# Kernel optimization log

Hardware: AMD Instinct MI355X
Metric: run time of the kernel (lower is better)

## Reference

```python
import jax, jax.numpy as jnp
import numpy as np

RES = 32  # voxel grid resolution per axis (cfg.MODEL.NEURAL_POINTS.VOXEL_RES)


def upsample_ac(x, s):
    """Bilinear upsample with align_corners=True. x: [B,C,h,w] -> [B,C,h*s,w*s]."""
    if s == 1:
        return x
    B, C, h, w = x.shape
    H, W = h * s, w * s
    ys = jnp.arange(H, dtype=x.dtype) * ((h - 1) / (H - 1))
    xs = jnp.arange(W, dtype=x.dtype) * ((w - 1) / (W - 1))
    y0 = jnp.floor(ys).astype(jnp.int32)
    x0 = jnp.floor(xs).astype(jnp.int32)
    y1 = jnp.minimum(y0 + 1, h - 1)
    x1 = jnp.minimum(x0 + 1, w - 1)
    wy = (ys - y0.astype(x.dtype))[:, None]  # [H,1]
    wx = (xs - x0.astype(x.dtype))[None, :]  # [1,W]
    top = x[:, :, y0, :]
    bot = x[:, :, y1, :]
    a = top[..., x0]; b = top[..., x1]; c = bot[..., x0]; d = bot[..., x1]
    return (a * (1 - wx) + b * wx) * (1 - wy) + (c * (1 - wx) + d * wx) * wy


def vox_closest(pos):
    """construct_vox_points_closest: per occupied voxel, index of point closest to
    the voxel's point centroid. pos: [N,3] -> [RES^3] int32 indices."""
    N = pos.shape[0]
    Vn = RES ** 3
    mn = pos.min(0)
    mx = pos.max(0)
    vsz = (mx - mn) / RES  # obtain_voxel_size_based_grid_res
    coord = jnp.clip(jnp.floor((pos - mn) / vsz).astype(jnp.int32), 0, RES - 1)
    vid = (coord[:, 0] * RES + coord[:, 1]) * RES + coord[:, 2]  # [N]
    cnt = jax.ops.segment_sum(jnp.ones((N,), pos.dtype), vid, Vn)
    cen = jax.ops.segment_sum(pos, vid, Vn) / jnp.maximum(cnt, 1.0)[:, None]
    d = jnp.sum((pos - cen[vid]) ** 2, axis=-1)  # [N] dist^2 to own-voxel centroid
    dmin = jax.ops.segment_min(d, vid, Vn)
    cand = jnp.where(d <= dmin[vid], jnp.arange(N, dtype=jnp.int32), N)
    midx = jax.ops.segment_min(cand, vid, Vn)
    return jnp.where(midx >= N, 0, midx)  # guard (rare) empty voxels


def reference(rgb, f1, f2, f3, points_pos, points_dir, W1, b1, W2, b2, points_mask):
    V, _, H, W = rgb.shape
    N = V * H * W
    C = 59
    # valid_index = where(points_mask == 1) (mask is all ones -> identity gather)
    valid = jnp.nonzero(points_mask[0] == 1, size=N, fill_value=0)[0]
    pos = points_pos[0, valid]          # [N,3]
    pdir = points_dir[0, valid]         # [N,3]
    # project_point_feats: upsample each pyramid level to full res, concat channels
    ups = [upsample_ac(rgb, 1), upsample_ac(f1, 2), upsample_ac(f2, 4), upsample_ac(f3, 8)]
    pif = jnp.concatenate(ups, axis=1)                       # [V,59,H,W]
    pif = jnp.transpose(pif, (0, 2, 3, 1)).reshape(N, C)     # [N,59]
    color = jax.lax.stop_gradient(jnp.transpose(rgb, (0, 2, 3, 1)).reshape(N, 3))
    pif = pif[valid]
    color = color[valid]
    emb = jnp.concatenate([pif, pdir], axis=-1)              # [N,62]
    midx = vox_closest(pos)                                  # [32768]
    sel_emb = emb[midx]
    sel_pos = pos[midx]
    sel_color = color[midx]
    sel_dir = pdir[midx]
    # point_mlp (premlp_init): 62 -> 256 -> 256
    h = jax.nn.relu(sel_emb @ W1 + b1)
    points_embedding = h @ W2 + b2
    return points_embedding, sel_pos, sel_color, sel_dir


def setup_inputs() -> dict:
    key = jax.random.key(0)
    ks = jax.random.split(key, 10)
    V, H, W = 8, 240, 320
    N = V * H * W
    return {
        "rgb": jax.random.uniform(ks[0], (V, 3, H, W), jnp.float32),
        "f1": jax.random.normal(ks[1], (V, 8, H // 2, W // 2), jnp.float32),
        "f2": jax.random.normal(ks[2], (V, 16, H // 4, W // 4), jnp.float32),
        "f3": jax.random.normal(ks[3], (V, 32, H // 8, W // 8), jnp.float32),
        "points_pos": jax.random.uniform(ks[4], (1, N, 3), jnp.float32),
        "points_dir": jax.random.normal(ks[5], (1, N, 3), jnp.float32),
        "W1": jax.random.normal(ks[6], (62, 256), jnp.float32) * 0.05,
        "b1": jnp.zeros((256,), jnp.float32),
        "W2": jax.random.normal(ks[7], (256, 256), jnp.float32) * 0.05,
        "b2": jnp.zeros((256,), jnp.float32),
        "points_mask": jnp.ones((1, N), jnp.int32),
    }
```

## Files before the change

kernel.cpp:

```cpp
#include <hip/hip_runtime.h>
#include <hip/hip_bf16.h>
#include <limits.h>
#include <stddef.h>

#define NPTS   614400
#define RESV   32
#define NVOX   (RESV*RESV*RESV)
#define IMG_H  240
#define IMG_W  320
#define IMG_HW (IMG_H*IMG_W)
#define INF    __builtin_inff()
#define CAP    64
#define CAPP   32
#define SPILLCAP 4096
#define NBKT   128
#define BCAP   6144
#define BOVFCAP 4096

typedef __attribute__((ext_vector_type(8))) short short8;
typedef __attribute__((ext_vector_type(4))) short s16x4;
typedef __attribute__((ext_vector_type(4))) float f32x4;
typedef float f32x4u __attribute__((ext_vector_type(4), aligned(4)));

__device__ __forceinline__ float fadd_(float a, float b){
#pragma clang fp contract(off)
  return a + b;
}
__device__ __forceinline__ float fsub_(float a, float b){
#pragma clang fp contract(off)
  return a - b;
}
__device__ __forceinline__ float fmul_(float a, float b){
#pragma clang fp contract(off)
  return a * b;
}
__device__ __forceinline__ float fdiv_(float a, float b){
#pragma clang fp contract(off)
  return a / b;
}

__device__ __forceinline__ short f2bf(float x){
  __hip_bfloat16 h = __float2bfloat16(x);
  return *reinterpret_cast<short*>(&h);
}

__global__ void k_prep(int* __restrict__ spillcnt, int* __restrict__ gbase,
                       const float* __restrict__ W1, const float* __restrict__ W2,
                       short* __restrict__ W1t, short* __restrict__ W2t,
                       const float* __restrict__ pos,
                       f32x4* __restrict__ pmin, f32x4* __restrict__ pmax){
  int gid = blockIdx.x*blockDim.x + threadIdx.x;
  int stride = gridDim.x*blockDim.x;
  if (gid == 0){ spillcnt[0] = 0; spillcnt[1] = 0; }
  if (gid < NBKT) gbase[gid] = 0;
  if (gid < 256*64){
    int n = gid >> 6, k = gid & 63;
    W1t[gid] = (k < 62) ? f2bf(W1[k*256 + n]) : (short)0;
  } else if (gid < 256*64 + 256*256){
    int j = gid - 256*64;
    int n = j >> 8, k = j & 255;
    W2t[j] = f2bf(W2[k*256 + n]);
  }

  const f32x4* p4 = (const f32x4*)pos;
  float mn[3] = {  INF,  INF,  INF };
  float mx[3] = { -INF, -INF, -INF };
  for (int t = gid; t < NPTS/4; t += stride){
    f32x4 a = p4[3*t+0], b = p4[3*t+1], c = p4[3*t+2];
    mn[0] = fminf(mn[0], fminf(fminf(a.x, a.w), fminf(b.z, c.y)));
    mx[0] = fmaxf(mx[0], fmaxf(fmaxf(a.x, a.w), fmaxf(b.z, c.y)));
    mn[1] = fminf(mn[1], fminf(fminf(a.y, b.x), fminf(b.w, c.z)));
    mx[1] = fmaxf(mx[1], fmaxf(fmaxf(a.y, b.x), fmaxf(b.w, c.z)));
    mn[2] = fminf(mn[2], fminf(fminf(a.z, b.y), fminf(c.x, c.w)));
    mx[2] = fmaxf(mx[2], fmaxf(fmaxf(a.z, b.y), fmaxf(c.x, c.w)));
  }
  #pragma unroll
  for (int off = 32; off >= 1; off >>= 1){
    #pragma unroll
    for (int c = 0; c < 3; c++){
      mn[c] = fminf(mn[c], __shfl_down(mn[c], off, 64));
      mx[c] = fmaxf(mx[c], __shfl_down(mx[c], off, 64));
    }
  }
  __shared__ float smn[4][3], smx[4][3];
  int lane = threadIdx.x & 63, w = threadIdx.x >> 6;
  if (lane == 0){
    #pragma unroll
    for (int c = 0; c < 3; c++){ smn[w][c] = mn[c]; smx[w][c] = mx[c]; }
  }
  __syncthreads();
  if (threadIdx.x == 0){
    f32x4 a, b;
    a.x = fminf(fminf(smn[0][0], smn[1][0]), fminf(smn[2][0], smn[3][0]));
    a.y = fminf(fminf(smn[0][1], smn[1][1]), fminf(smn[2][1], smn[3][1]));
    a.z = fminf(fminf(smn[0][2], smn[1][2]), fminf(smn[2][2], smn[3][2]));
    a.w = 0.f;
    b.x = fmaxf(fmaxf(smx[0][0], smx[1][0]), fmaxf(smx[2][0], smx[3][0]));
    b.y = fmaxf(fmaxf(smx[0][1], smx[1][1]), fmaxf(smx[2][1], smx[3][1]));
    b.z = fmaxf(fmaxf(smx[0][2], smx[1][2]), fmaxf(smx[2][2], smx[3][2]));
    b.w = 0.f;
    pmin[blockIdx.x] = a;
    pmax[blockIdx.x] = b;
  }
}

__device__ __forceinline__ void reduce_minmax(const f32x4* __restrict__ pmin,
                                              const f32x4* __restrict__ pmax,
                                              float mn[3], float vsz[3]){
  int t = threadIdx.x;
  f32x4 a = pmin[t], b = pmin[t+256];
  f32x4 c = pmax[t], d = pmax[t+256];
  float lmn[3] = { fminf(a.x,b.x), fminf(a.y,b.y), fminf(a.z,b.z) };
  float lmx[3] = { fmaxf(c.x,d.x), fmaxf(c.y,d.y), fmaxf(c.z,d.z) };
  #pragma unroll
  for (int off = 32; off >= 1; off >>= 1){
    #pragma unroll
    for (int k = 0; k < 3; k++){
      lmn[k] = fminf(lmn[k], __shfl_xor(lmn[k], off, 64));
      lmx[k] = fmaxf(lmx[k], __shfl_xor(lmx[k], off, 64));
    }
  }
  __shared__ float smn[4][3], smx[4][3];
  int lane = t & 63, w = t >> 6;
  if (lane == 0){
    #pragma unroll
    for (int k = 0; k < 3; k++){ smn[w][k] = lmn[k]; smx[w][k] = lmx[k]; }
  }
  __syncthreads();
  #pragma unroll
  for (int k = 0; k < 3; k++){
    mn[k] = fminf(fminf(smn[0][k], smn[1][k]), fminf(smn[2][k], smn[3][k]));
    float mx = fmaxf(fmaxf(smx[0][k], smx[1][k]), fmaxf(smx[2][k], smx[3][k]));
    vsz[k] = fdiv_(fsub_(mx, mn[k]), 32.0f);
  }
}

__global__ void k_bucket(const float* __restrict__ pos,
                         const f32x4* __restrict__ pmin, const f32x4* __restrict__ pmax,
                         int* __restrict__ gbase, f32x4* __restrict__ bucketbuf,
                         int* __restrict__ bovfcnt, f32x4* __restrict__ bovf,
                         const float* __restrict__ f1, const float* __restrict__ f2,
                         const float* __restrict__ f3,
                         float* __restrict__ f1t, float* __restrict__ f2t,
                         float* __restrict__ f3t, int tposed){
  float mn[3], vsz[3];
  reduce_minmax(pmin, pmax, mn, vsz);

  __shared__ int h[NBKT], cur[NBKT];
  int t = threadIdx.x;
  if (t < NBKT) h[t] = 0;
  __syncthreads();

  int base = blockIdx.x*blockDim.x + t;
  const f32x4* p4 = (const f32x4*)pos;
  f32x4 a = p4[3*base+0], b = p4[3*base+1], c = p4[3*base+2];
  float X[4] = {a.x, a.w, b.z, c.y};
  float Y[4] = {a.y, b.x, b.w, c.z};
  float Z[4] = {a.z, b.y, c.x, c.w};
  int vox[4];
  #pragma unroll
  for (int j = 0; j < 4; j++){
    float P[3] = {X[j], Y[j], Z[j]};
    int v = 0;
    #pragma unroll
    for (int k = 0; k < 3; k++){
      float tt = fdiv_(fsub_(P[k], mn[k]), vsz[k]);
      int cc = (int)floorf(tt);
      cc = min(max(cc, 0), RESV-1);
      v = v*RESV + cc;
    }
    vox[j] = v;
    atomicAdd(&h[v >> 8], 1);
  }
  __syncthreads();
  if (t < NBKT) cur[t] = atomicAdd(&gbase[t], h[t]);
  __syncthreads();
  #pragma unroll
  for (int j = 0; j < 4; j++){
    int i = 4*base + j;
    int bk = vox[j] >> 8;
    int r = atomicAdd(&cur[bk], 1);
    f32x4 e = { X[j], Y[j], Z[j], __int_as_float(i) };
    if (r < BCAP){
      bucketbuf[(size_t)bk*BCAP + r] = e;
    } else {
      int so = atomicAdd(bovfcnt, 1);
      if (so < BOVFCAP) bovf[so] = e;
    }
  }

  if (tposed){
    int gid = blockIdx.x*blockDim.x + t;
    int stride = gridDim.x*blockDim.x;
    for (int p = gid; p < 8*19200; p += stride){
      int img = p / 19200, pix = p - img*19200;
      const float* s = f1 + (size_t)img*8*19200 + pix;
      float r[8];
      #pragma unroll
      for (int c = 0; c < 8; c++) r[c] = s[(size_t)c*19200];
      float* d = f1t + (size_t)p*8;
      *(f32x4*)&d[0] = (f32x4){r[0],r[1],r[2],r[3]};
      *(f32x4*)&d[4] = (f32x4){r[4],r[5],r[6],r[7]};
    }
    for (int p = gid; p < 8*4800; p += stride){
      int img = p / 4800, pix = p - img*4800;
      const float* s = f2 + (size_t)img*16*4800 + pix;
      float* d = f2t + (size_t)p*16;
      #pragma unroll
      for (int cq = 0; cq < 4; cq++){
        f32x4 v = { s[(size_t)(4*cq+0)*4800], s[(size_t)(4*cq+1)*4800],
                    s[(size_t)(4*cq+2)*4800], s[(size_t)(4*cq+3)*4800] };
        *(f32x4*)&d[4*cq] = v;
      }
    }
    for (int p = gid; p < 8*1200; p += stride){
      int img = p / 1200, pix = p - img*1200;
      const float* s = f3 + (size_t)img*32*1200 + pix;
      float* d = f3t + (size_t)p*32;
      #pragma unroll
      for (int cq = 0; cq < 8; cq++){
        f32x4 v = { s[(size_t)(4*cq+0)*1200], s[(size_t)(4*cq+1)*1200],
                    s[(size_t)(4*cq+2)*1200], s[(size_t)(4*cq+3)*1200] };
        *(f32x4*)&d[4*cq] = v;
      }
    }
  }
}

__launch_bounds__(512)
__global__ void k_vox2(const f32x4* __restrict__ pmin, const f32x4* __restrict__ pmax,
                       const int* __restrict__ gbase, const f32x4* __restrict__ bucketbuf,
                       const int* __restrict__ bovfcnt, const f32x4* __restrict__ bovf,
                       int* __restrict__ cnt, int* __restrict__ slots,
                       int* __restrict__ spillcnt, int2* __restrict__ spill,
                       f32x4* __restrict__ slotpos, int haspp){
  __shared__ float smn[8][3], smx[8][3];
  __shared__ int cnt_s[256];
  int t = threadIdx.x;
  if (t < 256) cnt_s[t] = 0;

  {
    int tt = t & 255;
    f32x4 a = pmin[tt], b = pmin[tt+256];
    f32x4 c = pmax[tt], d = pmax[tt+256];
    float lmn[3] = { fminf(a.x,b.x), fminf(a.y,b.y), fminf(a.z,b.z) };
    float lmx[3] = { fmaxf(c.x,d.x), fmaxf(c.y,d.y), fmaxf(c.z,d.z) };
    #pragma unroll
    for (int off = 32; off >= 1; off >>= 1){
      #pragma unroll
      for (int k = 0; k < 3; k++){
        lmn[k] = fminf(lmn[k], __shfl_xor(lmn[k], off, 64));
        lmx[k] = fmaxf(lmx[k], __shfl_xor(lmx[k], off, 64));
      }
    }
    int lane = t & 63, w = t >> 6;
    if (lane == 0){
      #pragma unroll
      for (int k = 0; k < 3; k++){ smn[w][k] = lmn[k]; smx[w][k] = lmx[k]; }
    }
  }
  __syncthreads();
  float mn[3], vsz[3];
  #pragma unroll
  for (int k = 0; k < 3; k++){
    float lo = smn[0][k], hi = smx[0][k];
    #pragma unroll
    for (int w = 1; w < 8; w++){ lo = fminf(lo, smn[w][k]); hi = fmaxf(hi, smx[w][k]); }
    mn[k] = lo;
    vsz[k] = fdiv_(fsub_(hi, lo), 32.0f);
  }

  int b = blockIdx.x;
  int nb = min(gbase[b], BCAP);
  for (int j = t; j < nb; j += 512){
    f32x4 rec = bucketbuf[(size_t)b*BCAP + j];
    float P[3] = {rec.x, rec.y, rec.z};
    int v = 0;
    #pragma unroll
    for (int k = 0; k < 3; k++){
      float tt = fdiv_(fsub_(P[k], mn[k]), vsz[k]);
      int cc = (int)floorf(tt);
      cc = min(max(cc, 0), RESV-1);
      v = v*RESV + cc;
    }
    int p = atomicAdd(&cnt_s[v & 255], 1);
    if (haspp && p < CAPP){
      slotpos[(size_t)v*CAPP + p] = rec;
    } else if (p < CAP){
      slots[v*CAP + p] = __float_as_int(rec.w);
    } else {
      int sp = atomicAdd(spillcnt, 1);
      if (sp < SPILLCAP){ int2 e; e.x = v; e.y = __float_as_int(rec.w); spill[sp] = e; }
    }
  }
  int bc = min(*bovfcnt, BOVFCAP);
  for (int j = t; j < bc; j += 512){
    f32x4 rec = bovf[j];
    float P[3] = {rec.x, rec.y, rec.z};
    int v = 0;
    #pragma unroll
    for (int k = 0; k < 3; k++){
      float tt = fdiv_(fsub_(P[k], mn[k]), vsz[k]);
      int cc = (int)floorf(tt);
      cc = min(max(cc, 0), RESV-1);
      v = v*RESV + cc;
    }
    if ((v >> 8) == b){
      int p = atomicAdd(&cnt_s[v & 255], 1);
      if (haspp && p < CAPP){
        slotpos[(size_t)v*CAPP + p] = rec;
      } else if (p < CAP){
        slots[v*CAP + p] = __float_as_int(rec.w);
      } else {
        int sp = atomicAdd(spillcnt, 1);
        if (sp < SPILLCAP){ int2 e; e.x = v; e.y = __float_as_int(rec.w); spill[sp] = e; }
      }
    }
  }
  __syncthreads();
  if (t < 256) cnt[(b << 8) + t] = cnt_s[t];
}

__launch_bounds__(256)
__global__ void k_voxfull(const int* __restrict__ cnt, const int* __restrict__ slots,
                          const int* __restrict__ spillcnt, const int2* __restrict__ spill,
                          const f32x4* __restrict__ slotpos, int haspp,
                          const float* __restrict__ pos,
                          const float* __restrict__ pdir, const float* __restrict__ rgb,
                          const float* __restrict__ f1, const float* __restrict__ f2,
                          const float* __restrict__ f3,
                          const float* __restrict__ f1t, const float* __restrict__ f2t,
                          const float* __restrict__ f3t, int tposed,
                          float* __restrict__ selpos, float* __restrict__ selcol,
                          float* __restrict__ seldir, short* __restrict__ emb){
  __shared__ __align__(16) int skey[4][64];
  __shared__ f32x4 sposl[4][64];
  int lane = threadIdx.x & 63;
  int wv   = threadIdx.x >> 6;
  int v = blockIdx.x*4 + wv;

  f32x4 q = {0.f, 0.f, 0.f, 0.f};
  if (haspp) q = slotpos[(size_t)v*CAPP + (lane & (CAPP-1))];
  int n = cnt[v];

  int m = 0;
  unsigned long long ball = 0;
  float px = 0.f, py = 0.f, pz = 0.f;

  if (n > CAP){
    if (lane == 0){
      int sc = min(*spillcnt, SPILLCAP);
      float sx = 0.f, sy = 0.f, sz = 0.f; int last = -1;
      for (int i = 0; i < n; i++){
        int best = INT_MAX;
        for (int j = 0; j < CAP; j++){
          int id = (haspp && j < CAPP) ? __float_as_int(slotpos[(size_t)v*CAPP + j].w)
                                       : slots[v*CAP + j];
          if (id > last && id < best) best = id;
        }
        for (int j = 0; j < sc; j++){
          int2 e = spill[j];
          if (e.x == v && e.y > last && e.y < best) best = e.y;
        }
        sx = fadd_(sx, pos[3*best+0]);
        sy = fadd_(sy, pos[3*best+1]);
        sz = fadd_(sz, pos[3*best+2]);
        last = best;
      }
      float cf = (float)n;
      float cx = fdiv_(sx, cf), cy = fdiv_(sy, cf), cz = fdiv_(sz, cf);
      float dmin = INF; int mm = 0;
      for (int j = 0; j < CAP + sc; j++){
        int id; int ok = 1;
        if (j < CAP){
          id = (haspp && j < CAPP) ? __float_as_int(slotpos[(size_t)v*CAPP + j].w)
                                   : slots[v*CAP + j];
        } else { int2 e = spill[j-CAP]; ok = (e.x == v); id = e.y; }
        if (!ok) continue;
        float dx = fsub_(pos[3*id+0], cx);
        float dy = fsub_(pos[3*id+1], cy);
        float dz = fsub_(pos[3*id+2], cz);
        float d  = fadd_(fadd_(fmul_(dx,dx), fmul_(dy,dy)), fmul_(dz,dz));
        if (d < dmin || (d == dmin && id < mm)){ dmin = d; mm = id; }
      }
      m = mm;
    }
    m = __shfl(m, 0, 64);
  } else {
    int key = INT_MAX;
    if (haspp && n <= CAPP){
      if (lane < n){
        px = q.x; py = q.y; pz = q.z;
        key = __float_as_int(q.w);
      }
    } else if (haspp){
      if (lane < CAPP){
        px = q.x; py = q.y; pz = q.z;
        key = __float_as_int(q.w);
      } else if (lane < n){
        key = slots[v*CAP + lane];
        if (key < NPTS-1){
          f32x4u qq = *(const f32x4u*)&pos[3*key];
          px = qq.x; py = qq.y; pz = qq.z;
        } else {
          px = pos[3*key+0]; py = pos[3*key+1]; pz = pos[3*key+2];
        }
      }
    } else {
      if (lane < n){
        key = slots[v*CAP + lane];
        if (key < NPTS-1){
          f32x4u qq = *(const f32x4u*)&pos[3*key];
          px = qq.x; py = qq.y; pz = qq.z;
        } else {
          px = pos[3*key+0]; py = pos[3*key+1]; pz = pos[3*key+2];
        }
      }
    }

    skey[wv][lane] = key;
    __builtin_amdgcn_wave_barrier();
    int r = 0;
    {
      int nq = (n + 3) >> 2;
      const int4* k4 = (const int4*)&skey[wv][0];
      for (int j = 0; j < nq; j++){
        int4 kk = k4[j];
        r += (kk.x < key) + (kk.y < key) + (kk.z < key) + (kk.w < key);
      }
    }
    if (lane < n){
      f32x4 e = { px, py, pz, 0.f };
      sposl[wv][r] = e;
    }
    __builtin_amdgcn_wave_barrier();

    float sx = 0.f, sy = 0.f, sz = 0.f;
    for (int i = 0; i < n; i++){
      f32x4 pp = sposl[wv][i];
      sx = fadd_(sx, pp.x);
      sy = fadd_(sy, pp.y);
      sz = fadd_(sz, pp.z);
    }
    float cf = fmaxf((float)n, 1.0f);
    float cx = fdiv_(sx, cf), cy = fdiv_(sy, cf), cz = fdiv_(sz, cf);

    float bd = INF; int bi = 0;
    if (lane < n){
      float dx = fsub_(px, cx), dy = fsub_(py, cy), dz = fsub_(pz, cz);
      bd = fadd_(fadd_(fmul_(dx,dx), fmul_(dy,dy)), fmul_(dz,dz));
      bi = key;
    }
    #pragma unroll
    for (int off = 32; off >= 1; off >>= 1){
      float od = __shfl_xor(bd, off, 64);
      int   oi = __shfl_xor(bi, off, 64);
      if (od < bd || (od == bd && oi < bi)){ bd = od; bi = oi; }
    }
    m = bi;
    ball = __ballot(lane < n && key == m);
  }

  float wx_ = 0.f, wy_ = 0.f, wz_ = 0.f;
  if (ball){
    int wl = (int)(__ffsll((long long)ball) - 1);
    wx_ = __shfl(px, wl, 64);
    wy_ = __shfl(py, wl, 64);
    wz_ = __shfl(pz, wl, 64);
  }

  int img = m / IMG_HW;
  int rem = m - img*IMG_HW;
  int y = rem / IMG_W;
  int x = rem - y*IMG_W;
  int ch = lane;
  float val;
  if (ch < 3){
    val = rgb[((img*3 + ch)*IMG_H + y)*IMG_W + x];
    selcol[3*v+ch] = val;
    float sp = ball ? ((ch == 0) ? wx_ : (ch == 1) ? wy_ : wz_) : pos[3*m+ch];
    selpos[3*v+ch] = sp;
  } else if (ch < 59){
    int lvl = (ch >= 27) ? 2 : ((ch >= 11) ? 1 : 0);
    int c   = ch - ((lvl == 0) ? 3 : ((lvl == 1) ? 11 : 27));
    int C   = 8 << lvl;
    int h   = 120 >> lvl, w = 160 >> lvl;
    float ry = (lvl == 0) ? (119.0f/239.0f) : ((lvl == 1) ? (59.0f/239.0f) : (29.0f/239.0f));
    float rx = (lvl == 0) ? (159.0f/319.0f) : ((lvl == 1) ? (79.0f/319.0f) : (39.0f/319.0f));
    float ys = (float)y * ry;
    float xs = (float)x * rx;
    int y0 = (int)floorf(ys);
    int x0 = (int)floorf(xs);
    int y1 = min(y0+1, h-1);
    int x1 = min(x0+1, w-1);
    float wy = ys - (float)y0;
    float wx = xs - (float)x0;
    float aa, bb, cc, dd;
    if (tposed){
      const float* ft = (lvl == 0) ? f1t : ((lvl == 1) ? f2t : f3t);
      const float* base = ft + (size_t)(img*h*w)*C + c;
      aa = base[(y0*w + x0)*C];
      bb = base[(y0*w + x1)*C];
      cc = base[(y1*w + x0)*C];
      dd = base[(y1*w + x1)*C];
    } else {
      const float* f = (lvl == 0) ? f1 : ((lvl == 1) ? f2 : f3);
      const float* plane = f + ((size_t)img*C + c)*(size_t)(h*w);
      aa = plane[y0*w + x0];
      bb = plane[y0*w + x1];
      cc = plane[y1*w + x0];
      dd = plane[y1*w + x1];
    }
    val = (aa*(1.f-wx) + bb*wx)*(1.f-wy) + (cc*(1.f-wx) + dd*wx)*wy;
  } else if (ch < 62){
    val = pdir[3*m + (ch-59)];
    seldir[3*v+(ch-59)] = val;
  } else {
    val = 0.f;
  }
  emb[(size_t)v*64 + ch] = f2bf(val);
}

#define MLP_BLOCKS 512
#define MLP_TILES  (NVOX/16/MLP_BLOCKS)
__launch_bounds__(256, 2)
__global__ void k_mlp(const short* __restrict__ emb, const short* __restrict__ W1t,
                      const float* __restrict__ b1f, const short* __restrict__ W2t,
                      const float* __restrict__ b2f, float* __restrict__ out){
  __shared__ short Hs[16][264];
  int t    = threadIdx.x;
  int lane = t & 63;
  int wv   = t >> 6;
  int m    = lane & 15;
  int q    = lane >> 4;

  short8 w1f[4][2], w2f[4][8];
  float  b1r[4][4], b2r[4];
  #pragma unroll
  for (int nt = 0; nt < 4; nt++){
    int n = wv*64 + nt*16 + m;
    #pragma unroll
    for (int kq = 0; kq < 2; kq++)
      w1f[nt][kq] = *(const short8*)&W1t[(size_t)n*64 + kq*32 + q*8];
    #pragma unroll
    for (int kq = 0; kq < 8; kq++)
      w2f[nt][kq] = *(const short8*)&W2t[(size_t)n*256 + kq*32 + q*8];
    #pragma unroll
    for (int i = 0; i < 4; i++)
      b1r[nt][i] = b1f[wv*64 + nt*16 + q*4 + i];
    b2r[nt] = b2f[n];
  }

  for (int tt = 0; tt < MLP_TILES; tt++){
    int row0 = (blockIdx.x*MLP_TILES + tt)*16;

    short8 ef0 = *(const short8*)&emb[(size_t)(row0 + m)*64 + q*8];
    short8 ef1 = *(const short8*)&emb[(size_t)(row0 + m)*64 + 32 + q*8];

    #pragma unroll
    for (int nt = 0; nt < 4; nt++){
      f32x4 c = {0.f, 0.f, 0.f, 0.f};
      c = __builtin_amdgcn_mfma_f32_16x16x32_bf16(w1f[nt][0], ef0, c, 0, 0, 0);
      c = __builtin_amdgcn_mfma_f32_16x16x32_bf16(w1f[nt][1], ef1, c, 0, 0, 0);
      s16x4 hv;
      #pragma unroll
      for (int i = 0; i < 4; i++)
        hv[i] = f2bf(fmaxf(c[i] + b1r[nt][i], 0.f));
      *(s16x4*)&Hs[m][wv*64 + nt*16 + q*4] = hv;
    }
    __syncthreads();

    f32x4 acc[4] = {{0,0,0,0},{0,0,0,0},{0,0,0,0},{0,0,0,0}};
    #pragma unroll
    for (int kq = 0; kq < 8; kq++){
      short8 af = *(const short8*)&Hs[m][kq*32 + q*8];
      #pragma unroll
      for (int nt = 0; nt < 4; nt++)
        acc[nt] = __builtin_amdgcn_mfma_f32_16x16x32_bf16(af, w2f[nt][kq], acc[nt], 0, 0, 0);
    }
    __syncthreads();

    #pragma unroll
    for (int nt = 0; nt < 4; nt++){
      int n = wv*64 + nt*16 + m;
      #pragma unroll
      for (int i = 0; i < 4; i++)
        out[(size_t)(row0 + q*4 + i)*256 + n] = acc[nt][i] + b2r[nt];
    }
  }
}

extern "C" void kernel_launch(void* const* d_in, const int* in_sizes, int n_in,
                              void* d_out, int out_size, void* d_ws, size_t ws_size,
                              hipStream_t stream){
  const float* rgb  = (const float*)d_in[0];
  const float* f1   = (const float*)d_in[1];
  const float* f2   = (const float*)d_in[2];
  const float* f3   = (const float*)d_in[3];
  const float* pos  = (const float*)d_in[4];
  const float* pdir = (const float*)d_in[5];
  const float* W1   = (const float*)d_in[6];
  const float* b1   = (const float*)d_in[7];
  const float* W2   = (const float*)d_in[8];
  const float* b2   = (const float*)d_in[9];

  float* out      = (float*)d_out;
  float* out_emb  = out;
  float* out_pos  = out + (size_t)NVOX*256;
  float* out_col  = out_pos + (size_t)NVOX*3;
  float* out_dir  = out_col + (size_t)NVOX*3;

  char* ob = (char*)out_emb;
  f32x4* bucketbuf = (f32x4*)ob;
  f32x4* bovf      = (f32x4*)(ob + (size_t)NBKT*BCAP*16);
  int*   gbase     = (int*)  (ob + (size_t)NBKT*BCAP*16 + (size_t)BOVFCAP*16);

  char* w = (char*)d_ws;
  int*   spillcnt = (int*)w;       w += 64;
  f32x4* pmin     = (f32x4*)w;     w += (size_t)512*16;
  f32x4* pmax     = (f32x4*)w;     w += (size_t)512*16;
  int*   cnt      = (int*)w;       w += (size_t)NVOX*4;
  short* W1t      = (short*)w;     w += (size_t)256*64*2;
  short* W2t      = (short*)w;     w += (size_t)256*256*2;
  short* emb      = (short*)w;     w += (size_t)NVOX*64*2;
  int2*  spill    = (int2*)w;      w += (size_t)SPILLCAP*8;
  int*   slots    = (int*)w;       w += (size_t)NVOX*CAP*4;
  float* f1t      = (float*)w;     w += (size_t)8*19200*8*4;
  float* f2t      = (float*)w;     w += (size_t)8*4800*16*4;
  float* f3t      = (float*)w;     w += (size_t)8*1200*32*4;
  int tposed = ((size_t)(w - (char*)d_ws) <= ws_size) ? 1 : 0;
  f32x4* slotpos  = (f32x4*)w;     w += (size_t)NVOX*CAPP*16;
  int haspp = ((size_t)(w - (char*)d_ws) <= ws_size) ? 1 : 0;

  int* bovfcnt = spillcnt + 1;

  k_prep   <<<512,       256, 0, stream>>>(spillcnt, gbase, W1, W2, W1t, W2t,
                                           pos, pmin, pmax);
  k_bucket <<<NPTS/1024, 256, 0, stream>>>(pos, pmin, pmax, gbase, bucketbuf,
                                           bovfcnt, bovf,
                                           f1, f2, f3, f1t, f2t, f3t, tposed);
  k_vox2   <<<NBKT,      512, 0, stream>>>(pmin, pmax, gbase, bucketbuf, bovfcnt, bovf,
                                           cnt, slots, spillcnt, spill, slotpos, haspp);
  k_voxfull<<<NVOX/4,    256, 0, stream>>>(cnt, slots, spillcnt, spill, slotpos, haspp,
                                           pos, pdir, rgb, f1, f2, f3,
                                           f1t, f2t, f3t, tposed,
                                           out_pos, out_col, out_dir, emb);
  k_mlp    <<<MLP_BLOCKS,256, 0, stream>>>(emb, W1t, b1, W2t, b2, out_emb);
}
```

Baseline: 174.1 us.

## Fuse voxel scatter and per-voxel selection into one kernel with shared-memory payloads

Merges the bucket-to-voxel scatter kernel and the per-voxel closest-point/feature kernel into a single kernel. Each block owns 64 voxels (buckets go from 128 of 256 voxels to 512 of 64 voxels) and keeps up to 32 point records per voxel in shared memory instead of writing them to a global slot-position buffer. This removes a kernel launch plus the global round-trips for counts and slot positions. The overflow path now rescans the bucket instead of using a spill list. The cost is only 512 blocks of 512 threads, each serially processing 8 voxels per wave, with heavy LDS use, so occupancy and parallelism drop.

```diff
diff --git a/kernel.cpp b/kernel.cpp
--- a/kernel.cpp
+++ b/kernel.cpp
@@ -12,9 +12,8 @@
 #define INF    __builtin_inff()
 #define CAP    64
 #define CAPP   32
-#define SPILLCAP 4096
-#define NBKT   128
-#define BCAP   6144
+#define NBKT   512
+#define BCAP   2048
 #define BOVFCAP 4096
 
 typedef __attribute__((ext_vector_type(8))) short short8;
@@ -44,14 +43,27 @@
   return *reinterpret_cast<short*>(&h);
 }
 
-__global__ void k_prep(int* __restrict__ spillcnt, int* __restrict__ gbase,
+__device__ __forceinline__ int voxid_of(f32x4 rec, const float mn[3], const float vsz[3]){
+  float P[3] = {rec.x, rec.y, rec.z};
+  int v = 0;
+  #pragma unroll
+  for (int k = 0; k < 3; k++){
+    float tt = fdiv_(fsub_(P[k], mn[k]), vsz[k]);
+    int cc = (int)floorf(tt);
+    cc = min(max(cc, 0), RESV-1);
+    v = v*RESV + cc;
+  }
+  return v;
+}
+
+__global__ void k_prep(int* __restrict__ counters, int* __restrict__ gbase,
                        const float* __restrict__ W1, const float* __restrict__ W2,
                        short* __restrict__ W1t, short* __restrict__ W2t,
                        const float* __restrict__ pos,
                        f32x4* __restrict__ pmin, f32x4* __restrict__ pmax){
   int gid = blockIdx.x*blockDim.x + threadIdx.x;
   int stride = gridDim.x*blockDim.x;
-  if (gid == 0){ spillcnt[0] = 0; spillcnt[1] = 0; }
+  if (gid == 0) counters[0] = 0;
   if (gid < NBKT) gbase[gid] = 0;
   if (gid < 256*64){
     int n = gid >> 6, k = gid & 63;
@@ -148,7 +160,7 @@
 
   __shared__ int h[NBKT], cur[NBKT];
   int t = threadIdx.x;
-  if (t < NBKT) h[t] = 0;
+  for (int i = t; i < NBKT; i += 256) h[i] = 0;
   __syncthreads();
 
   int base = blockIdx.x*blockDim.x + t;
@@ -160,25 +172,19 @@
   int vox[4];
   #pragma unroll
   for (int j = 0; j < 4; j++){
-    float P[3] = {X[j], Y[j], Z[j]};
-    int v = 0;
-    #pragma unroll
-    for (int k = 0; k < 3; k++){
-      float tt = fdiv_(fsub_(P[k], mn[k]), vsz[k]);
-      int cc = (int)floorf(tt);
-      cc = min(max(cc, 0), RESV-1);
-      v = v*RESV + cc;
-    }
+    f32x4 e = { X[j], Y[j], Z[j], 0.f };
+    int v = voxid_of(e, mn, vsz);
     vox[j] = v;
-    atomicAdd(&h[v >> 8], 1);
-  }
-  __syncthreads();
-  if (t < NBKT) cur[t] = atomicAdd(&gbase[t], h[t]);
+    atomicAdd(&h[v >> 6], 1);
+  }
+  __syncthreads();
+  for (int i = t; i < NBKT; i += 256)
+    cur[i] = atomicAdd(&gbase[i], h[i]);
   __syncthreads();
   #pragma unroll
   for (int j = 0; j < 4; j++){
     int i = 4*base + j;
-    int bk = vox[j] >> 8;
+    int bk = vox[j] >> 6;
     int r = atomicAdd(&cur[bk], 1);
     f32x4 e = { X[j], Y[j], Z[j], __int_as_float(i) };
     if (r < BCAP){
@@ -197,7 +203,7 @@
       const float* s = f1 + (size_t)img*8*19200 + pix;
       float r[8];
       #pragma unroll
-      for (int c = 0; c < 8; c++) r[c] = s[(size_t)c*19200];
+      for (int cc = 0; cc < 8; cc++) r[cc] = s[(size_t)cc*19200];
       float* d = f1t + (size_t)p*8;
       *(f32x4*)&d[0] = (f32x4){r[0],r[1],r[2],r[3]};
       *(f32x4*)&d[4] = (f32x4){r[4],r[5],r[6],r[7]};
@@ -228,16 +234,26 @@
 }
 
 __launch_bounds__(512)
-__global__ void k_vox2(const f32x4* __restrict__ pmin, const f32x4* __restrict__ pmax,
+__global__ void k_voxf(const f32x4* __restrict__ pmin, const f32x4* __restrict__ pmax,
                        const int* __restrict__ gbase, const f32x4* __restrict__ bucketbuf,
                        const int* __restrict__ bovfcnt, const f32x4* __restrict__ bovf,
-                       int* __restrict__ cnt, int* __restrict__ slots,
-                       int* __restrict__ spillcnt, int2* __restrict__ spill,
-                       f32x4* __restrict__ slotpos, int haspp){
+                       int* __restrict__ slots,
+                       const float* __restrict__ pos,
+                       const float* __restrict__ pdir, const float* __restrict__ rgb,
+                       const float* __restrict__ f1, const float* __restrict__ f2,
+                       const float* __restrict__ f3,
+                       const float* __restrict__ f1t, const float* __restrict__ f2t,
+                       const float* __restrict__ f3t, int tposed,
+                       float* __restrict__ selpos, float* __restrict__ selcol,
+                       float* __restrict__ seldir, short* __restrict__ emb){
   __shared__ float smn[8][3], smx[8][3];
-  __shared__ int cnt_s[256];
+  __shared__ int cnt_s[64];
+  __shared__ f32x4 pay[64][CAPP];
+  __shared__ __align__(16) int skey[8][64];
+  __shared__ f32x4 sposl[8][64];
   int t = threadIdx.x;
-  if (t < 256) cnt_s[t] = 0;
+  int lane = t & 63, wv = t >> 6;
+  if (t < 64) cnt_s[t] = 0;
 
   {
     int tt = t & 255;
@@ -253,10 +269,9 @@
         lmx[k] = fmaxf(lmx[k], __shfl_xor(lmx[k], off, 64));
       }
     }
-    int lane = t & 63, w = t >> 6;
     if (lane == 0){
       #pragma unroll
-      for (int k = 0; k < 3; k++){ smn[w][k] = lmn[k]; smx[w][k] = lmx[k]; }
+      for (int k = 0; k < 3; k++){ smn[wv][k] = lmn[k]; smx[wv][k] = lmx[k]; }
     }
   }
   __syncthreads();
@@ -270,131 +285,69 @@
     vsz[k] = fdiv_(fsub_(hi, lo), 32.0f);
   }
 
-  int b = blockIdx.x;
+  int b  = blockIdx.x;
   int nb = min(gbase[b], BCAP);
+  int bc = min(*bovfcnt, BOVFCAP);
+
   for (int j = t; j < nb; j += 512){
     f32x4 rec = bucketbuf[(size_t)b*BCAP + j];
-    float P[3] = {rec.x, rec.y, rec.z};
-    int v = 0;
-    #pragma unroll
-    for (int k = 0; k < 3; k++){
-      float tt = fdiv_(fsub_(P[k], mn[k]), vsz[k]);
-      int cc = (int)floorf(tt);
-      cc = min(max(cc, 0), RESV-1);
-      v = v*RESV + cc;
-    }
-    int p = atomicAdd(&cnt_s[v & 255], 1);
-    if (haspp && p < CAPP){
-      slotpos[(size_t)v*CAPP + p] = rec;
-    } else if (p < CAP){
-      slots[v*CAP + p] = __float_as_int(rec.w);
-    } else {
-      int sp = atomicAdd(spillcnt, 1);
-      if (sp < SPILLCAP){ int2 e; e.x = v; e.y = __float_as_int(rec.w); spill[sp] = e; }
-    }
-  }
-  int bc = min(*bovfcnt, BOVFCAP);
+    int v = voxid_of(rec, mn, vsz);
+    int vloc = v & 63;
+    int p = atomicAdd(&cnt_s[vloc], 1);
+    if (p < CAPP)      pay[vloc][p] = rec;
+    else if (p < CAP)  slots[v*CAP + p] = __float_as_int(rec.w);
+  }
   for (int j = t; j < bc; j += 512){
     f32x4 rec = bovf[j];
-    float P[3] = {rec.x, rec.y, rec.z};
-    int v = 0;
-    #pragma unroll
-    for (int k = 0; k < 3; k++){
-      float tt = fdiv_(fsub_(P[k], mn[k]), vsz[k]);
-      int cc = (int)floorf(tt);
-      cc = min(max(cc, 0), RESV-1);
-      v = v*RESV + cc;
-    }
-    if ((v >> 8) == b){
-      int p = atomicAdd(&cnt_s[v & 255], 1);
-      if (haspp && p < CAPP){
-        slotpos[(size_t)v*CAPP + p] = rec;
-      } else if (p < CAP){
-        slots[v*CAP + p] = __float_as_int(rec.w);
-      } else {
-        int sp = atomicAdd(spillcnt, 1);
-        if (sp < SPILLCAP){ int2 e; e.x = v; e.y = __float_as_int(rec.w); spill[sp] = e; }
-      }
-    }
-  }
-  __syncthreads();
-  if (t < 256) cnt[(b << 8) + t] = cnt_s[t];
-}
-
-__launch_bounds__(256)
-__global__ void k_voxfull(const int* __restrict__ cnt, const int* __restrict__ slots,
-                          const int* __restrict__ spillcnt, const int2* __restrict__ spill,
-                          const f32x4* __restrict__ slotpos, int haspp,
-                          const float* __restrict__ pos,
-                          const float* __restrict__ pdir, const float* __restrict__ rgb,
-                          const float* __restrict__ f1, const float* __restrict__ f2,
-                          const float* __restrict__ f3,
-                          const float* __restrict__ f1t, const float* __restrict__ f2t,
-                          const float* __restrict__ f3t, int tposed,
-                          float* __restrict__ selpos, float* __restrict__ selcol,
-                          float* __restrict__ seldir, short* __restrict__ emb){
-  __shared__ __align__(16) int skey[4][64];
-  __shared__ f32x4 sposl[4][64];
-  int lane = threadIdx.x & 63;
-  int wv   = threadIdx.x >> 6;
-  int v = blockIdx.x*4 + wv;
-
-  f32x4 q = {0.f, 0.f, 0.f, 0.f};
-  if (haspp) q = slotpos[(size_t)v*CAPP + (lane & (CAPP-1))];
-  int n = cnt[v];
-
-  int m = 0;
-  unsigned long long ball = 0;
-  float px = 0.f, py = 0.f, pz = 0.f;
-
-  if (n > CAP){
-    if (lane == 0){
-      int sc = min(*spillcnt, SPILLCAP);
-      float sx = 0.f, sy = 0.f, sz = 0.f; int last = -1;
-      for (int i = 0; i < n; i++){
-        int best = INT_MAX;
-        for (int j = 0; j < CAP; j++){
-          int id = (haspp && j < CAPP) ? __float_as_int(slotpos[(size_t)v*CAPP + j].w)
-                                       : slots[v*CAP + j];
-          if (id > last && id < best) best = id;
+    int v = voxid_of(rec, mn, vsz);
+    if ((v >> 6) != b) continue;
+    int vloc = v & 63;
+    int p = atomicAdd(&cnt_s[vloc], 1);
+    if (p < CAPP)      pay[vloc][p] = rec;
+    else if (p < CAP)  slots[v*CAP + p] = __float_as_int(rec.w);
+  }
+  __syncthreads();
+
+  for (int i = 0; i < 8; i++){
+    int vloc = wv*8 + i;
+    int v = (b << 6) + vloc;
+    int n = cnt_s[vloc];
+    int m = 0;
+    unsigned long long ball = 0;
+    float px = 0.f, py = 0.f, pz = 0.f;
+
+    if (n > CAP){
+      if (lane == 0){
+        float sx = 0.f, sy = 0.f, sz = 0.f; int last = -1;
+        for (int it = 0; it < n; it++){
+          int best = INT_MAX; f32x4 bp = {0.f,0.f,0.f,0.f};
+          for (int j = 0; j < nb + bc; j++){
+            f32x4 rec = (j < nb) ? bucketbuf[(size_t)b*BCAP + j] : bovf[j-nb];
+            if (voxid_of(rec, mn, vsz) != v) continue;
+            int id = __float_as_int(rec.w);
+            if (id > last && id < best){ best = id; bp = rec; }
+          }
+          sx = fadd_(sx, bp.x); sy = fadd_(sy, bp.y); sz = fadd_(sz, bp.z);
+          last = best;
         }
-        for (int j = 0; j < sc; j++){
-          int2 e = spill[j];
-          if (e.x == v && e.y > last && e.y < best) best = e.y;
+        float cf = (float)n;
+        float cx = fdiv_(sx, cf), cy = fdiv_(sy, cf), cz = fdiv_(sz, cf);
+        float dmin = INF; int mm = 0;
+        for (int j = 0; j < nb + bc; j++){
+          f32x4 rec = (j < nb) ? bucketbuf[(size_t)b*BCAP + j] : bovf[j-nb];
+          if (voxid_of(rec, mn, vsz) != v) continue;
+          int id = __float_as_int(rec.w);
+          float dx = fsub_(rec.x, cx), dy = fsub_(rec.y, cy), dz = fsub_(rec.z, cz);
+          float d  = fadd_(fadd_(fmul_(dx,dx), fmul_(dy,dy)), fmul_(dz,dz));
+          if (d < dmin || (d == dmin && id < mm)){ dmin = d; mm = id; }
         }
-        sx = fadd_(sx, pos[3*best+0]);
-        sy = fadd_(sy, pos[3*best+1]);
-        sz = fadd_(sz, pos[3*best+2]);
-        last = best;
-      }
-      float cf = (float)n;
-      float cx = fdiv_(sx, cf), cy = fdiv_(sy, cf), cz = fdiv_(sz, cf);
-      float dmin = INF; int mm = 0;
-      for (int j = 0; j < CAP + sc; j++){
-        int id; int ok = 1;
-        if (j < CAP){
-          id = (haspp && j < CAPP) ? __float_as_int(slotpos[(size_t)v*CAPP + j].w)
-                                   : slots[v*CAP + j];
-        } else { int2 e = spill[j-CAP]; ok = (e.x == v); id = e.y; }
-        if (!ok) continue;
-        float dx = fsub_(pos[3*id+0], cx);
-        float dy = fsub_(pos[3*id+1], cy);
-        float dz = fsub_(pos[3*id+2], cz);
-        float d  = fadd_(fadd_(fmul_(dx,dx), fmul_(dy,dy)), fmul_(dz,dz));
-        if (d < dmin || (d == dmin && id < mm)){ dmin = d; mm = id; }
-      }
-      m = mm;
-    }
-    m = __shfl(m, 0, 64);
-  } else {
-    int key = INT_MAX;
-    if (haspp && n <= CAPP){
-      if (lane < n){
-        px = q.x; py = q.y; pz = q.z;
-        key = __float_as_int(q.w);
-      }
-    } else if (haspp){
-      if (lane < CAPP){
+        m = mm;
+      }
+      m = __shfl(m, 0, 64);
+    } else {
+      int key = INT_MAX;
+      if (lane < n && lane < CAPP){
+        f32x4 q = pay[vloc][lane];
         px = q.x; py = q.y; pz = q.z;
         key = __float_as_int(q.w);
       } else if (lane < n){
@@ -406,119 +359,110 @@
           px = pos[3*key+0]; py = pos[3*key+1]; pz = pos[3*key+2];
         }
       }
+
+      skey[wv][lane] = key;
+      __builtin_amdgcn_wave_barrier();
+      int r = 0;
+      {
+        int nq = (n + 3) >> 2;
+        const int4* k4 = (const int4*)&skey[wv][0];
+        for (int j = 0; j < nq; j++){
+          int4 kk = k4[j];
+          r += (kk.x < key) + (kk.y < key) + (kk.z < key) + (kk.w < key);
+        }
+      }
+      if (lane < n){
+        f32x4 e = { px, py, pz, 0.f };
+        sposl[wv][r] = e;
+      }
+      __builtin_amdgcn_wave_barrier();
+
+      float sx = 0.f, sy = 0.f, sz = 0.f;
+      for (int j = 0; j < n; j++){
+        f32x4 pp = sposl[wv][j];
+        sx = fadd_(sx, pp.x);
+        sy = fadd_(sy, pp.y);
+        sz = fadd_(sz, pp.z);
+      }
+      float cf = fmaxf((float)n, 1.0f);
+      float cx = fdiv_(sx, cf), cy = fdiv_(sy, cf), cz = fdiv_(sz, cf);
+
+      float bd = INF; int bi = 0;
+      if (lane < n){
+        float dx = fsub_(px, cx), dy = fsub_(py, cy), dz = fsub_(pz, cz);
+        bd = fadd_(fadd_(fmul_(dx,dx), fmul_(dy,dy)), fmul_(dz,dz));
+        bi = key;
+      }
+      #pragma unroll
+      for (int off = 32; off >= 1; off >>= 1){
+        float od = __shfl_xor(bd, off, 64);
+        int   oi = __shfl_xor(bi, off, 64);
+        if (od < bd || (od == bd && oi < bi)){ bd = od; bi = oi; }
+      }
+      m = bi;
+      ball = __ballot(lane < n && key == m);
+    }
+
+    float wx_ = 0.f, wy_ = 0.f, wz_ = 0.f;
+    if (ball){
+      int wl = (int)(__ffsll((long long)ball) - 1);
+      wx_ = __shfl(px, wl, 64);
+      wy_ = __shfl(py, wl, 64);
+      wz_ = __shfl(pz, wl, 64);
+    }
+
+    int img = m / IMG_HW;
+    int rem = m - img*IMG_HW;
+    int y = rem / IMG_W;
+    int x = rem - y*IMG_W;
+    int ch = lane;
+    float val;
+    if (ch < 3){
+      val = rgb[((img*3 + ch)*IMG_H + y)*IMG_W + x];
+      selcol[3*v+ch] = val;
+      float sp = ball ? ((ch == 0) ? wx_ : (ch == 1) ? wy_ : wz_) : pos[3*m+ch];
+      selpos[3*v+ch] = sp;
+    } else if (ch < 59){
+      int lvl = (ch >= 27) ? 2 : ((ch >= 11) ? 1 : 0);
+      int c   = ch - ((lvl == 0) ? 3 : ((lvl == 1) ? 11 : 27));
+      int C   = 8 << lvl;
+      int h   = 120 >> lvl, w = 160 >> lvl;
+      float ry = (lvl == 0) ? (119.0f/239.0f) : ((lvl == 1) ? (59.0f/239.0f) : (29.0f/239.0f));
+      float rx = (lvl == 0) ? (159.0f/319.0f) : ((lvl == 1) ? (79.0f/319.0f) : (39.0f/319.0f));
+      float ys = (float)y * ry;
+      float xs = (float)x * rx;
+      int y0 = (int)floorf(ys);
+      int x0 = (int)floorf(xs);
+      int y1 = min(y0+1, h-1);
+      int x1 = min(x0+1, w-1);
+      float wy = ys - (float)y0;
+      float wx = xs - (float)x0;
+      float aa, bb, cc, dd;
+      if (tposed){
+        const float* ft = (lvl == 0) ? f1t : ((lvl == 1) ? f2t : f3t);
+        const float* base = ft + (size_t)(img*h*w)*C + c;
+        aa = base[(y0*w + x0)*C];
+        bb = base[(y0*w + x1)*C];
+        cc = base[(y1*w + x0)*C];
+        dd = base[(y1*w + x1)*C];
+      } else {
+        const float* f = (lvl == 0) ? f1 : ((lvl == 1) ? f2 : f3);
+        const float* plane = f + ((size_t)img*C + c)*(size_t)(h*w);
+        aa = plane[y0*w + x0];
+        bb = plane[y0*w + x1];
+        cc = plane[y1*w + x0];
+        dd = plane[y1*w + x1];
+      }
+      val = (aa*(1.f-wx) + bb*wx)*(1.f-wy) + (cc*(1.f-wx) + dd*wx)*wy;
+    } else if (ch < 62){
+      val = pdir[3*m + (ch-59)];
+      seldir[3*v+(ch-59)] = val;
     } else {
-      if (lane < n){
-        key = slots[v*CAP + lane];
-        if (key < NPTS-1){
-          f32x4u qq = *(const f32x4u*)&pos[3*key];
-          px = qq.x; py = qq.y; pz = qq.z;
-        } else {
-          px = pos[3*key+0]; py = pos[3*key+1]; pz = pos[3*key+2];
-        }
-      }
-    }
-
-    skey[wv][lane] = key;
+      val = 0.f;
+    }
+    emb[(size_t)v*64 + ch] = f2bf(val);
     __builtin_amdgcn_wave_barrier();
-    int r = 0;
-    {
-      int nq = (n + 3) >> 2;
-      const int4* k4 = (const int4*)&skey[wv][0];
-      for (int j = 0; j < nq; j++){
-        int4 kk = k4[j];
-        r += (kk.x < key) + (kk.y < key) + (kk.z < key) + (kk.w < key);
-      }
-    }
-    if (lane < n){
-      f32x4 e = { px, py, pz, 0.f };
-      sposl[wv][r] = e;
-    }
-    __builtin_amdgcn_wave_barrier();
-
-    float sx = 0.f, sy = 0.f, sz = 0.f;
-    for (int i = 0; i < n; i++){
-      f32x4 pp = sposl[wv][i];
-      sx = fadd_(sx, pp.x);
-      sy = fadd_(sy, pp.y);
-      sz = fadd_(sz, pp.z);
-    }
-    float cf = fmaxf((float)n, 1.0f);
-    float cx = fdiv_(sx, cf), cy = fdiv_(sy, cf), cz = fdiv_(sz, cf);
-
-    float bd = INF; int bi = 0;
-    if (lane < n){
-      float dx = fsub_(px, cx), dy = fsub_(py, cy), dz = fsub_(pz, cz);
-      bd = fadd_(fadd_(fmul_(dx,dx), fmul_(dy,dy)), fmul_(dz,dz));
-      bi = key;
-    }
-    #pragma unroll
-    for (int off = 32; off >= 1; off >>= 1){
-      float od = __shfl_xor(bd, off, 64);
-      int   oi = __shfl_xor(bi, off, 64);
-      if (od < bd || (od == bd && oi < bi)){ bd = od; bi = oi; }
-    }
-    m = bi;
-    ball = __ballot(lane < n && key == m);
-  }
-
-  float wx_ = 0.f, wy_ = 0.f, wz_ = 0.f;
-  if (ball){
-    int wl = (int)(__ffsll((long long)ball) - 1);
-    wx_ = __shfl(px, wl, 64);
-    wy_ = __shfl(py, wl, 64);
-    wz_ = __shfl(pz, wl, 64);
-  }
-
-  int img = m / IMG_HW;
-  int rem = m - img*IMG_HW;
-  int y = rem / IMG_W;
-  int x = rem - y*IMG_W;
-  int ch = lane;
-  float val;
-  if (ch < 3){
-    val = rgb[((img*3 + ch)*IMG_H + y)*IMG_W + x];
-    selcol[3*v+ch] = val;
-    float sp = ball ? ((ch == 0) ? wx_ : (ch == 1) ? wy_ : wz_) : pos[3*m+ch];
-    selpos[3*v+ch] = sp;
-  } else if (ch < 59){
-    int lvl = (ch >= 27) ? 2 : ((ch >= 11) ? 1 : 0);
-    int c   = ch - ((lvl == 0) ? 3 : ((lvl == 1) ? 11 : 27));
-    int C   = 8 << lvl;
-    int h   = 120 >> lvl, w = 160 >> lvl;
-    float ry = (lvl == 0) ? (119.0f/239.0f) : ((lvl == 1) ? (59.0f/239.0f) : (29.0f/239.0f));
-    float rx = (lvl == 0) ? (159.0f/319.0f) : ((lvl == 1) ? (79.0f/319.0f) : (39.0f/319.0f));
-    float ys = (float)y * ry;
-    float xs = (float)x * rx;
-    int y0 = (int)floorf(ys);
-    int x0 = (int)floorf(xs);
-    int y1 = min(y0+1, h-1);
-    int x1 = min(x0+1, w-1);
-    float wy = ys - (float)y0;
-    float wx = xs - (float)x0;
-    float aa, bb, cc, dd;
-    if (tposed){
-      const float* ft = (lvl == 0) ? f1t : ((lvl == 1) ? f2t : f3t);
-      const float* base = ft + (size_t)(img*h*w)*C + c;
-      aa = base[(y0*w + x0)*C];
-      bb = base[(y0*w + x1)*C];
-      cc = base[(y1*w + x0)*C];
-      dd = base[(y1*w + x1)*C];
-    } else {
-      const float* f = (lvl == 0) ? f1 : ((lvl == 1) ? f2 : f3);
-      const float* plane = f + ((size_t)img*C + c)*(size_t)(h*w);
-      aa = plane[y0*w + x0];
-      bb = plane[y0*w + x1];
-      cc = plane[y1*w + x0];
-      dd = plane[y1*w + x1];
-    }
-    val = (aa*(1.f-wx) + bb*wx)*(1.f-wy) + (cc*(1.f-wx) + dd*wx)*wy;
-  } else if (ch < 62){
-    val = pdir[3*m + (ch-59)];
-    seldir[3*v+(ch-59)] = val;
-  } else {
-    val = 0.f;
-  }
-  emb[(size_t)v*64 + ch] = f2bf(val);
+  }
 }
 
 #define MLP_BLOCKS 512
@@ -616,33 +560,27 @@
   int*   gbase     = (int*)  (ob + (size_t)NBKT*BCAP*16 + (size_t)BOVFCAP*16);
 
   char* w = (char*)d_ws;
-  int*   spillcnt = (int*)w;       w += 64;
+  int*   counters = (int*)w;       w += 64;
   f32x4* pmin     = (f32x4*)w;     w += (size_t)512*16;
   f32x4* pmax     = (f32x4*)w;     w += (size_t)512*16;
-  int*   cnt      = (int*)w;       w += (size_t)NVOX*4;
   short* W1t      = (short*)w;     w += (size_t)256*64*2;
   short* W2t      = (short*)w;     w += (size_t)256*256*2;
   short* emb      = (short*)w;     w += (size_t)NVOX*64*2;
-  int2*  spill    = (int2*)w;      w += (size_t)SPILLCAP*8;
   int*   slots    = (int*)w;       w += (size_t)NVOX*CAP*4;
   float* f1t      = (float*)w;     w += (size_t)8*19200*8*4;
   float* f2t      = (float*)w;     w += (size_t)8*4800*16*4;
   float* f3t      = (float*)w;     w += (size_t)8*1200*32*4;
   int tposed = ((size_t)(w - (char*)d_ws) <= ws_size) ? 1 : 0;
-  f32x4* slotpos  = (f32x4*)w;     w += (size_t)NVOX*CAPP*16;
-  int haspp = ((size_t)(w - (char*)d_ws) <= ws_size) ? 1 : 0;
-
-  int* bovfcnt = spillcnt + 1;
-
-  k_prep   <<<512,       256, 0, stream>>>(spillcnt, gbase, W1, W2, W1t, W2t,
+
+  int* bovfcnt = counters;
+
+  k_prep   <<<512,       256, 0, stream>>>(counters, gbase, W1, W2, W1t, W2t,
                                            pos, pmin, pmax);
   k_bucket <<<NPTS/1024, 256, 0, stream>>>(pos, pmin, pmax, gbase, bucketbuf,
                                            bovfcnt, bovf,
                                            f1, f2, f3, f1t, f2t, f3t, tposed);
-  k_vox2   <<<NBKT,      512, 0, stream>>>(pmin, pmax, gbase, bucketbuf, bovfcnt, bovf,
-                                           cnt, slots, spillcnt, spill, slotpos, haspp);
-  k_voxfull<<<NVOX/4,    256, 0, stream>>>(cnt, slots, spillcnt, spill, slotpos, haspp,
-                                           pos, pdir, rgb, f1, f2, f3,
+  k_voxf   <<<NBKT,      512, 0, stream>>>(pmin, pmax, gbase, bucketbuf, bovfcnt, bovf,
+                                           slots, pos, pdir, rgb, f1, f2, f3,
                                            f1t, f2t, f3t, tposed,
                                            out_pos, out_col, out_dir, emb);
   k_mlp    <<<MLP_BLOCKS,256, 0, stream>>>(emb, W1t, b1, W2t, b2, out_emb);
```

New measurement: 181.3 us. 4.1% more time.
